# Optimization experiments

Measured on AMD Instinct MI355X. Metric: run time of the kernel, lower is better.

## Reference

```python
import jax, jax.numpy as jnp
import numpy as np

N_NODES = 100000
N_EDGES = 1600000
IN_F, HID_F, OUT_F = 64, 64, 16


def setup_inputs() -> dict:
    key = jax.random.key(0)
    k_x, k_e, k_w1, k_w2 = jax.random.split(key, 4)
    x = jax.random.normal(k_x, (N_NODES, IN_F), dtype=jnp.float32)
    edge_index = jax.random.randint(k_e, (2, N_EDGES), 0, N_NODES, dtype=jnp.int64)
    # Glorot-ish init for the GCNConv linear weights; bias zeros (PyG default)
    W1 = jax.random.normal(k_w1, (IN_F, HID_F), dtype=jnp.float32) / np.sqrt(IN_F)
    b1 = jnp.zeros((HID_F,), dtype=jnp.float32)
    W2 = jax.random.normal(k_w2, (HID_F, OUT_F), dtype=jnp.float32) / np.sqrt(HID_F)
    b2 = jnp.zeros((OUT_F,), dtype=jnp.float32)
    return {"x": x, "edge_index": edge_index, "W1": W1, "b1": b1, "W2": W2, "b2": b2}


def reference(x, edge_index, W1, b1, W2, b2):
    N = x.shape[0]
    # GCNConv: add self-loops, symmetric normalization D^-1/2 A D^-1/2
    loop = jnp.arange(N, dtype=edge_index.dtype)
    src = jnp.concatenate([edge_index[0], loop])  # [E+N]
    dst = jnp.concatenate([edge_index[1], loop])  # [E+N]
    deg = jax.ops.segment_sum(jnp.ones_like(dst, dtype=x.dtype), dst, num_segments=N)
    dis = jax.lax.rsqrt(deg)  # deg >= 1 due to self-loops
    norm = dis[src] * dis[dst]  # [E+N]

    def gcn_conv(h, W, b):
        h = h @ W                                   # [N, d_out]
        msg = h[src] * norm[:, None]                # gather + scale  [E+N, d_out]
        agg = jax.ops.segment_sum(msg, dst, num_segments=N)  # scatter-add
        return agg + b

    h = jax.nn.relu(gcn_conv(x, W1, b1))
    h = gcn_conv(h, W2, b2)
    return jax.nn.log_softmax(h, axis=1)
```

## Files before the change

kernel.cpp:

```cpp
#include <hip/hip_runtime.h>
#include <hip/hip_bf16.h>
#include <hip/hip_fp16.h>


#define F1 64
#define F2 16
#define NBKT 256
#define BSH 512
#define NSB 256
#define SBD 1024
#define STG 9216

typedef _Float16 f16x8 __attribute__((ext_vector_type(8)));
typedef _Float16 f16x4 __attribute__((ext_vector_type(4)));
typedef _Float16 f16x2 __attribute__((ext_vector_type(2)));
typedef float f32x4 __attribute__((ext_vector_type(4)));

__device__ inline f16x8 shfl_xor_f16x8(f16x8 v, int off) {
  union U { f16x8 h; int i[4]; } a, b;
  a.h = v;
#pragma unroll
  for (int k = 0; k < 4; ++k) b.i[k] = __shfl_xor(a.i[k], off);
  return b.h;
}
__device__ inline f16x4 shfl_xor_f16x4(f16x4 v, int off) {
  union U { f16x4 h; int i[2]; } a, b;
  a.h = v;
#pragma unroll
  for (int k = 0; k < 2; ++k) b.i[k] = __shfl_xor(a.i[k], off);
  return b.h;
}

__global__ void k_scatterL(const int* __restrict__ src, const int* __restrict__ dst,
                           int* __restrict__ tmp, int* __restrict__ segstart,
                           int* __restrict__ bcnt, int E, int nb, int chunk,
                           const float* __restrict__ W1, const float* __restrict__ W2,
                           __half* __restrict__ W1T, __half* __restrict__ W2T) {
  int t = threadIdx.x, sb = blockIdx.x;
  if (sb == NSB) {
    for (int i = t; i < 64 * 64; i += SBD) {
      int n = i >> 6, k = i & 63;
      W1T[i] = __float2half(W1[k * 64 + n]);
    }
    for (int i = t; i < 16 * 64; i += SBD) {
      int n = i >> 6, k = i & 63;
      W2T[i] = __float2half(W2[k * 16 + n]);
    }
    return;
  }
  __shared__ int h[NBKT];
  __shared__ int cur[NBKT];
  __shared__ int sc[NBKT];
  int beg = sb * chunk, end = min(beg + chunk, E);
  for (int i = t; i < NBKT; i += SBD) h[i] = 0;
  __syncthreads();
  int e;
  for (e = beg + t * 4; e + 4 <= end; e += 4 * SBD) {
    int4 d4 = *(const int4*)(dst + e);
    atomicAdd(&h[d4.x >> 9], 1);
    atomicAdd(&h[d4.y >> 9], 1);
    atomicAdd(&h[d4.z >> 9], 1);
    atomicAdd(&h[d4.w >> 9], 1);
  }
  for (; e < end; ++e) atomicAdd(&h[dst[e] >> 9], 1);
  __syncthreads();
  for (int i = t; i < nb; i += SBD)
    if (h[i]) atomicAdd(&bcnt[i], h[i]);
  if (t < NBKT) sc[t] = h[t];
  __syncthreads();
  for (int off = 1; off < NBKT; off <<= 1) {
    int a = (t < NBKT && t >= off) ? sc[t - off] : 0;
    __syncthreads();
    if (t < NBKT) sc[t] += a;
    __syncthreads();
  }
  if (t < NBKT) cur[t] = (t == 0) ? 0 : sc[t - 1];
  __syncthreads();
  for (int i = t; i < nb; i += SBD) segstart[sb * (nb + 1) + i] = beg + cur[i];
  if (t == 0) segstart[sb * (nb + 1) + nb] = end;
  __syncthreads();
  for (e = beg + t * 4; e + 4 <= end; e += 4 * SBD) {
    int4 d4 = *(const int4*)(dst + e);
    int4 s4 = *(const int4*)(src + e);
    int b, off;
    b = d4.x >> 9; off = atomicAdd(&cur[b], 1); tmp[beg + off] = (s4.x << 9) | (d4.x & 511);
    b = d4.y >> 9; off = atomicAdd(&cur[b], 1); tmp[beg + off] = (s4.y << 9) | (d4.y & 511);
    b = d4.z >> 9; off = atomicAdd(&cur[b], 1); tmp[beg + off] = (s4.z << 9) | (d4.z & 511);
    b = d4.w >> 9; off = atomicAdd(&cur[b], 1); tmp[beg + off] = (s4.w << 9) | (d4.w & 511);
  }
  for (; e < end; ++e) {
    int d = dst[e];
    int b = d >> 9;
    int off = atomicAdd(&cur[b], 1);
    tmp[beg + off] = (src[e] << 9) | (d & 511);
  }
}

__global__ void k_csr(const int* __restrict__ tmp, const int* __restrict__ segstart,
                      const int* __restrict__ bcnt, int* __restrict__ csr,
                      int* __restrict__ rowptr, float* __restrict__ dis,
                      int N, int nb) {
  __shared__ int stage[STG];
  __shared__ int sc[BSH];
  __shared__ int cnt[BSH];
  __shared__ int lofs[BSH];
  __shared__ int s_beg;
  int b = blockIdx.x, t = threadIdx.x;
  sc[t] = (t < b) ? bcnt[t] : 0;
  __syncthreads();
  for (int off = 1; off < BSH; off <<= 1) {
    int a = (t >= off) ? sc[t - off] : 0;
    __syncthreads();
    sc[t] += a;
    __syncthreads();
  }
  if (t == 0) s_beg = sc[BSH - 1];
  __syncthreads();
  int beg = s_beg;
  int s0 = 0, len = 0;
  if (t < NSB) {
    s0 = segstart[t * (nb + 1) + b];
    len = segstart[t * (nb + 1) + b + 1] - s0;
  }
  sc[t] = (t < NSB) ? len : 0;
  __syncthreads();
  for (int off = 1; off < NSB; off <<= 1) {
    int a = (t < NSB && t >= off) ? sc[t - off] : 0;
    __syncthreads();
    if (t < NSB) sc[t] += a;
    __syncthreads();
  }
  int total = sc[NSB - 1];
  int my0 = (t == 0) ? 0 : ((t < NSB) ? sc[t - 1] : 0);
  if (t < NSB) {
    int i = 0;
    for (; i + 4 <= len; i += 4) {
      int v0 = tmp[s0 + i], v1 = tmp[s0 + i + 1], v2 = tmp[s0 + i + 2], v3 = tmp[s0 + i + 3];
      stage[my0 + i] = v0; stage[my0 + i + 1] = v1;
      stage[my0 + i + 2] = v2; stage[my0 + i + 3] = v3;
    }
    for (; i < len; ++i) stage[my0 + i] = tmp[s0 + i];
  }
  cnt[t] = 0;
  __syncthreads();
  for (int i = t; i < total; i += BSH) atomicAdd(&cnt[stage[i] & (BSH - 1)], 1);
  __syncthreads();
  sc[t] = cnt[t];
  __syncthreads();
  for (int off = 1; off < BSH; off <<= 1) {
    int a = (t >= off) ? sc[t - off] : 0;
    __syncthreads();
    sc[t] += a;
    __syncthreads();
  }
  int excl = (t == 0) ? 0 : sc[t - 1];
  lofs[t] = excl;
  int n = b * BSH + t;
  if (n <= N) rowptr[n] = beg + excl;
  if (n < N) dis[n] = rsqrtf((float)(cnt[t] + 1));
  cnt[t] = 0;
  __syncthreads();
  for (int i = t; i < total; i += BSH) {
    int p = stage[i];
    int l = p & (BSH - 1);
    int off = atomicAdd(&cnt[l], 1);
    csr[beg + lofs[l] + off] = p >> 9;
  }
}

__global__ void k_gemm1(const float* __restrict__ x, const __half* __restrict__ W1T,
                        const float* __restrict__ dis, __half* __restrict__ out, int N) {
  int t = threadIdx.x;
  int wv = t >> 6, lane = t & 63;
  int m = lane & 15, q = lane >> 4;
  int row0 = blockIdx.x * 64 + wv * 16;
  int arow = min(row0 + m, N - 1);
  const _Float16* wt = (const _Float16*)W1T;
  f16x8 bf[4][2];
#pragma unroll
  for (int c = 0; c < 4; ++c)
#pragma unroll
    for (int kt = 0; kt < 2; ++kt)
      bf[c][kt] = *(const f16x8*)&wt[(c * 16 + m) * 64 + kt * 32 + q * 8];
  f16x8 a[2];
#pragma unroll
  for (int kt = 0; kt < 2; ++kt) {
    const float4* xp = (const float4*)(x + (size_t)arow * 64 + kt * 32 + q * 8);
    float4 u = xp[0], v = xp[1];
    a[kt][0] = (_Float16)u.x; a[kt][1] = (_Float16)u.y;
    a[kt][2] = (_Float16)u.z; a[kt][3] = (_Float16)u.w;
    a[kt][4] = (_Float16)v.x; a[kt][5] = (_Float16)v.y;
    a[kt][6] = (_Float16)v.z; a[kt][7] = (_Float16)v.w;
  }
  f32x4 acc[4] = {};
#pragma unroll
  for (int kt = 0; kt < 2; ++kt)
#pragma unroll
    for (int c = 0; c < 4; ++c)
      acc[c] = __builtin_amdgcn_mfma_f32_16x16x32_f16(a[kt], bf[c][kt], acc[c], 0, 0, 0);
#pragma unroll
  for (int r = 0; r < 4; ++r) {
    int n = row0 + q * 4 + r;
    if (n < N) {
      float dn = dis[n];
#pragma unroll
      for (int c = 0; c < 4; ++c)
        out[(size_t)n * 64 + c * 16 + m] = __float2half(acc[c][r] * dn);
    }
  }
}

__global__ void k_agg1f(const __half* __restrict__ h, const float* __restrict__ dis,
                        const int* __restrict__ rowptr, const int* __restrict__ csr,
                        const float* __restrict__ b1, const __half* __restrict__ W2T,
                        __half* __restrict__ h2, int N) {
  int gt = blockIdx.x * blockDim.x + threadIdx.x;
  int n = gt >> 6;
  if (n >= N) return;
  int lane = gt & 63;
  int fl = lane & 7;
  int sub = lane >> 3;
  const _Float16* hp = (const _Float16*)h;
  float dn = dis[n];
  float4 bu = *(const float4*)(b1 + fl * 8);
  float4 bv = *(const float4*)(b1 + fl * 8 + 4);
  const _Float16* wt = (const _Float16*)W2T;
  f16x8 w0 = *(const f16x8*)&wt[(sub * 2 + 0) * 64 + fl * 8];
  f16x8 w1 = *(const f16x8*)&wt[(sub * 2 + 1) * 64 + fl * 8];
  f16x8 acc0 = {}, acc1 = {};
  if (sub == 0)
    acc0 = *(const f16x8*)&hp[(size_t)n * 64 + fl * 8];
  int beg = rowptr[n], end = rowptr[n + 1];
  int e = beg + sub;
  int sA = (e < end) ? csr[e] : -1;
  int sB = (e + 8 < end) ? csr[e + 8] : -1;
  while (sB >= 0) {
    int e2 = e + 16;
    int sC = (e2 < end) ? csr[e2] : -1;
    int sD = (e2 + 8 < end) ? csr[e2 + 8] : -1;
    f16x8 v0 = *(const f16x8*)&hp[(size_t)sA * 64 + fl * 8];
    f16x8 v1 = *(const f16x8*)&hp[(size_t)sB * 64 + fl * 8];
    acc0 += v0;
    acc1 += v1;
    sA = sC; sB = sD; e = e2;
  }
  if (sA >= 0)
    acc0 += *(const f16x8*)&hp[(size_t)sA * 64 + fl * 8];
  f16x8 acc = acc0 + acc1;
  acc += shfl_xor_f16x8(acc, 8);
  acc += shfl_xor_f16x8(acc, 16);
  acc += shfl_xor_f16x8(acc, 32);
  float bb[8] = {bu.x, bu.y, bu.z, bu.w, bv.x, bv.y, bv.z, bv.w};
  f16x8 hr16;
#pragma unroll
  for (int k = 0; k < 8; ++k)
    hr16[k] = (_Float16)fmaxf(fmaf(dn, (float)acc[k], bb[k]), 0.f);
  const f16x2* h2v = (const f16x2*)&hr16;
  const f16x2* w0v = (const f16x2*)&w0;
  const f16x2* w1v = (const f16x2*)&w1;
  f16x2 q0 = {}, q1 = {};
#pragma unroll
  for (int k = 0; k < 4; ++k) {
    q0 += h2v[k] * w0v[k];
    q1 += h2v[k] * w1v[k];
  }
  float p0 = (float)q0[0] + (float)q0[1];
  float p1 = (float)q1[0] + (float)q1[1];
  p0 += __shfl_xor(p0, 1); p1 += __shfl_xor(p1, 1);
  p0 += __shfl_xor(p0, 2); p1 += __shfl_xor(p1, 2);
  p0 += __shfl_xor(p0, 4); p1 += __shfl_xor(p1, 4);
  if (fl == 0) {
    __half2 o;
    o.x = __float2half(p0 * dn);
    o.y = __float2half(p1 * dn);
    *(__half2*)((_Float16*)h2 + (size_t)n * 16 + sub * 2) = o;
  }
}

__global__ void k_agg2(const __half* __restrict__ h2, const float* __restrict__ dis,
                       const int* __restrict__ rowptr, const int* __restrict__ csr,
                       const float* __restrict__ b2, float* __restrict__ out, int N) {
  int gt = blockIdx.x * blockDim.x + threadIdx.x;
  int n = gt >> 6;
  if (n >= N) return;
  int lane = gt & 63;
  int fl = lane & 3;
  int sub = lane >> 2;
  const _Float16* hp = (const _Float16*)h2;
  f16x4 acc0 = {}, acc1 = {};
  if (sub == 0)
    acc0 = *(const f16x4*)&hp[(size_t)n * 16 + fl * 4];
  int beg = rowptr[n], end = rowptr[n + 1];
  int e = beg + sub;
  int sA = (e < end) ? csr[e] : -1;
  int sB = (e + 16 < end) ? csr[e + 16] : -1;
  while (sB >= 0) {
    int e2 = e + 32;
    int sC = (e2 < end) ? csr[e2] : -1;
    int sD = (e2 + 16 < end) ? csr[e2 + 16] : -1;
    f16x4 v0 = *(const f16x4*)&hp[(size_t)sA * 16 + fl * 4];
    f16x4 v1 = *(const f16x4*)&hp[(size_t)sB * 16 + fl * 4];
    acc0 += v0;
    acc1 += v1;
    sA = sC; sB = sD; e = e2;
  }
  if (sA >= 0)
    acc0 += *(const f16x4*)&hp[(size_t)sA * 16 + fl * 4];
  f16x4 acc = acc0 + acc1;
  acc += shfl_xor_f16x4(acc, 4);
  acc += shfl_xor_f16x4(acc, 8);
  acc += shfl_xor_f16x4(acc, 16);
  acc += shfl_xor_f16x4(acc, 32);
  if (sub == 0) {
    float dn = dis[n];
    float4 bb = *(const float4*)(b2 + fl * 4);
    float v0 = fmaf(dn, (float)acc[0], bb.x);
    float v1 = fmaf(dn, (float)acc[1], bb.y);
    float v2 = fmaf(dn, (float)acc[2], bb.z);
    float v3 = fmaf(dn, (float)acc[3], bb.w);
    float m = fmaxf(fmaxf(v0, v1), fmaxf(v2, v3));
    m = fmaxf(m, __shfl_xor(m, 1));
    m = fmaxf(m, __shfl_xor(m, 2));
    float s2 = __expf(v0 - m) + __expf(v1 - m) + __expf(v2 - m) + __expf(v3 - m);
    s2 += __shfl_xor(s2, 1);
    s2 += __shfl_xor(s2, 2);
    float ls = m + __logf(s2);
    float4 o = {v0 - ls, v1 - ls, v2 - ls, v3 - ls};
    *(float4*)(out + (size_t)n * 16 + fl * 4) = o;
  }
}

extern "C" void kernel_launch(void* const* d_in, const int* in_sizes, int n_in,
                              void* d_out, int out_size, void* d_ws, size_t ws_size,
                              hipStream_t stream) {
  const float* x = (const float*)d_in[0];
  const int* ei = (const int*)d_in[1];
  const float* W1 = (const float*)d_in[2];
  const float* b1 = (const float*)d_in[3];
  const float* W2 = (const float*)d_in[4];
  const float* b2 = (const float*)d_in[5];
  float* out = (float*)d_out;

  int N = in_sizes[0] / F1;
  int E = in_sizes[1] / 2;
  const int* src = ei;
  const int* dst = ei + E;
  int nb = (N + BSH - 1) >> 9;
  int chunk = ((E + NSB - 1) / NSB + 3) & ~3;

  char* ws = (char*)d_ws;
  size_t o_bcnt  = 0;
  size_t o_w1t   = o_bcnt + NBKT * 4;
  size_t o_w2t   = o_w1t + 64 * 64 * 2;
  size_t o_seg   = (o_w2t + 16 * 64 * 2 + 255) & ~(size_t)255;
  size_t o_dis   = (o_seg + (size_t)NSB * (nb + 1) * 4 + 255) & ~(size_t)255;
  size_t o_rowp  = (o_dis + (size_t)N * 4 + 255) & ~(size_t)255;
  size_t o_tmp   = (o_rowp + (size_t)(N + 1) * 4 + 255) & ~(size_t)255;
  size_t o_csr   = (o_tmp + (size_t)NSB * chunk * 4 + 255) & ~(size_t)255;
  size_t o_h1    = (o_csr + (size_t)E * 4 + 255) & ~(size_t)255;
  size_t o_h2    = (o_h1 + (size_t)N * 64 * 2 + 255) & ~(size_t)255;

  int* bcnt    = (int*)(ws + o_bcnt);
  __half* W1T  = (__half*)(ws + o_w1t);
  __half* W2T  = (__half*)(ws + o_w2t);
  int* segst   = (int*)(ws + o_seg);
  float* dis   = (float*)(ws + o_dis);
  int* rowptr  = (int*)(ws + o_rowp);
  int* tmp     = (int*)(ws + o_tmp);
  int* csr     = (int*)(ws + o_csr);
  __half* h1   = (__half*)(ws + o_h1);
  __half* h2   = (__half*)(ws + o_h2);

  hipMemsetAsync(bcnt, 0, NBKT * 4, stream);

  k_scatterL<<<NSB + 1, SBD, 0, stream>>>(src, dst, tmp, segst, bcnt, E, nb, chunk,
                                          W1, W2, W1T, W2T);
  k_csr<<<nb, BSH, 0, stream>>>(tmp, segst, bcnt, csr, rowptr, dis, N, nb);

  int gb = (N + 63) / 64;
  k_gemm1<<<gb, 256, 0, stream>>>(x, W1T, dis, h1, N);
  k_agg1f<<<((size_t)N * 64 + 255) / 256, 256, 0, stream>>>(h1, dis, rowptr, csr, b1, W2T, h2, N);
  k_agg2<<<((size_t)N * 64 + 255) / 256, 256, 0, stream>>>(h2, dis, rowptr, csr, b2, out, N);
}
```

Before: 200.7 us.

## Pack two nodes per wavefront in aggregation and derive bucket offsets from segstart

The two aggregation kernels now give each node half a wavefront (32 lanes) instead of a full one, so each wave handles two nodes. This halves the grid size and the shuffle-reduction depth, at the cost of fewer parallel edge lanes per node. Separately, the global per-bucket count array, its memset and its atomics are removed. k_csr instead recovers each bucket's global start by reducing segstart offsets minus each chunk base, which cuts one memset launch and the global atomic traffic.

```diff
diff --git a/kernel.cpp b/kernel.cpp
--- a/kernel.cpp
+++ b/kernel.cpp
@@ -33,7 +33,7 @@
 
 __global__ void k_scatterL(const int* __restrict__ src, const int* __restrict__ dst,
                            int* __restrict__ tmp, int* __restrict__ segstart,
-                           int* __restrict__ bcnt, int E, int nb, int chunk,
+                           int E, int nb, int chunk,
                            const float* __restrict__ W1, const float* __restrict__ W2,
                            __half* __restrict__ W1T, __half* __restrict__ W2T) {
   int t = threadIdx.x, sb = blockIdx.x;
@@ -64,8 +64,6 @@
   }
   for (; e < end; ++e) atomicAdd(&h[dst[e] >> 9], 1);
   __syncthreads();
-  for (int i = t; i < nb; i += SBD)
-    if (h[i]) atomicAdd(&bcnt[i], h[i]);
   if (t < NBKT) sc[t] = h[t];
   __syncthreads();
   for (int off = 1; off < NBKT; off <<= 1) {
@@ -97,31 +95,28 @@
 }
 
 __global__ void k_csr(const int* __restrict__ tmp, const int* __restrict__ segstart,
-                      const int* __restrict__ bcnt, int* __restrict__ csr,
-                      int* __restrict__ rowptr, float* __restrict__ dis,
-                      int N, int nb) {
+                      int* __restrict__ csr, int* __restrict__ rowptr,
+                      float* __restrict__ dis, int N, int nb, int chunk) {
   __shared__ int stage[STG];
   __shared__ int sc[BSH];
   __shared__ int cnt[BSH];
   __shared__ int lofs[BSH];
   __shared__ int s_beg;
   int b = blockIdx.x, t = threadIdx.x;
-  sc[t] = (t < b) ? bcnt[t] : 0;
-  __syncthreads();
-  for (int off = 1; off < BSH; off <<= 1) {
-    int a = (t >= off) ? sc[t - off] : 0;
-    __syncthreads();
-    sc[t] += a;
-    __syncthreads();
-  }
-  if (t == 0) s_beg = sc[BSH - 1];
-  __syncthreads();
-  int beg = s_beg;
   int s0 = 0, len = 0;
   if (t < NSB) {
     s0 = segstart[t * (nb + 1) + b];
     len = segstart[t * (nb + 1) + b + 1] - s0;
   }
+  sc[t] = (t < NSB) ? (s0 - t * chunk) : 0;
+  __syncthreads();
+  for (int off = BSH / 2; off > 0; off >>= 1) {
+    if (t < off) sc[t] += sc[t + off];
+    __syncthreads();
+  }
+  if (t == 0) s_beg = sc[0];
+  __syncthreads();
+  int beg = s_beg;
   sc[t] = (t < NSB) ? len : 0;
   __syncthreads();
   for (int off = 1; off < NSB; off <<= 1) {
@@ -215,21 +210,86 @@
                         const float* __restrict__ b1, const __half* __restrict__ W2T,
                         __half* __restrict__ h2, int N) {
   int gt = blockIdx.x * blockDim.x + threadIdx.x;
-  int n = gt >> 6;
+  int w = gt >> 6;
+  int lane = gt & 63;
+  int half = lane >> 5;
+  int sub = (lane >> 3) & 3;
+  int fl = lane & 7;
+  int n = w * 2 + half;
   if (n >= N) return;
-  int lane = gt & 63;
-  int fl = lane & 7;
-  int sub = lane >> 3;
   const _Float16* hp = (const _Float16*)h;
   float dn = dis[n];
   float4 bu = *(const float4*)(b1 + fl * 8);
   float4 bv = *(const float4*)(b1 + fl * 8 + 4);
   const _Float16* wt = (const _Float16*)W2T;
-  f16x8 w0 = *(const f16x8*)&wt[(sub * 2 + 0) * 64 + fl * 8];
-  f16x8 w1 = *(const f16x8*)&wt[(sub * 2 + 1) * 64 + fl * 8];
+  f16x8 wj[4];
+#pragma unroll
+  for (int i = 0; i < 4; ++i)
+    wj[i] = *(const f16x8*)&wt[(sub * 4 + i) * 64 + fl * 8];
   f16x8 acc0 = {}, acc1 = {};
   if (sub == 0)
     acc0 = *(const f16x8*)&hp[(size_t)n * 64 + fl * 8];
+  int beg = rowptr[n], end = rowptr[n + 1];
+  int e = beg + sub;
+  int sA = (e < end) ? csr[e] : -1;
+  int sB = (e + 4 < end) ? csr[e + 4] : -1;
+  while (sB >= 0) {
+    int e2 = e + 8;
+    int sC = (e2 < end) ? csr[e2] : -1;
+    int sD = (e2 + 4 < end) ? csr[e2 + 4] : -1;
+    f16x8 v0 = *(const f16x8*)&hp[(size_t)sA * 64 + fl * 8];
+    f16x8 v1 = *(const f16x8*)&hp[(size_t)sB * 64 + fl * 8];
+    acc0 += v0;
+    acc1 += v1;
+    sA = sC; sB = sD; e = e2;
+  }
+  if (sA >= 0)
+    acc0 += *(const f16x8*)&hp[(size_t)sA * 64 + fl * 8];
+  f16x8 acc = acc0 + acc1;
+  acc += shfl_xor_f16x8(acc, 8);
+  acc += shfl_xor_f16x8(acc, 16);
+  float bb[8] = {bu.x, bu.y, bu.z, bu.w, bv.x, bv.y, bv.z, bv.w};
+  f16x8 hr16;
+#pragma unroll
+  for (int k = 0; k < 8; ++k)
+    hr16[k] = (_Float16)fmaxf(fmaf(dn, (float)acc[k], bb[k]), 0.f);
+  const f16x2* h2v = (const f16x2*)&hr16;
+  float p[4];
+#pragma unroll
+  for (int i = 0; i < 4; ++i) {
+    const f16x2* wv = (const f16x2*)&wj[i];
+    f16x2 qq = {};
+#pragma unroll
+    for (int k = 0; k < 4; ++k) qq += h2v[k] * wv[k];
+    float pi = (float)qq[0] + (float)qq[1];
+    pi += __shfl_xor(pi, 1);
+    pi += __shfl_xor(pi, 2);
+    pi += __shfl_xor(pi, 4);
+    p[i] = pi;
+  }
+  if (fl == 0) {
+    f16x4 o;
+#pragma unroll
+    for (int i = 0; i < 4; ++i) o[i] = (_Float16)(p[i] * dn);
+    *(f16x4*)((_Float16*)h2 + (size_t)n * 16 + sub * 4) = o;
+  }
+}
+
+__global__ void k_agg2(const __half* __restrict__ h2, const float* __restrict__ dis,
+                       const int* __restrict__ rowptr, const int* __restrict__ csr,
+                       const float* __restrict__ b2, float* __restrict__ out, int N) {
+  int gt = blockIdx.x * blockDim.x + threadIdx.x;
+  int w = gt >> 6;
+  int lane = gt & 63;
+  int half = lane >> 5;
+  int sub = (lane >> 2) & 7;
+  int fl = lane & 3;
+  int n = w * 2 + half;
+  if (n >= N) return;
+  const _Float16* hp = (const _Float16*)h2;
+  f16x4 acc0 = {}, acc1 = {};
+  if (sub == 0)
+    acc0 = *(const f16x4*)&hp[(size_t)n * 16 + fl * 4];
   int beg = rowptr[n], end = rowptr[n + 1];
   int e = beg + sub;
   int sA = (e < end) ? csr[e] : -1;
@@ -238,66 +298,6 @@
     int e2 = e + 16;
     int sC = (e2 < end) ? csr[e2] : -1;
     int sD = (e2 + 8 < end) ? csr[e2 + 8] : -1;
-    f16x8 v0 = *(const f16x8*)&hp[(size_t)sA * 64 + fl * 8];
-    f16x8 v1 = *(const f16x8*)&hp[(size_t)sB * 64 + fl * 8];
-    acc0 += v0;
-    acc1 += v1;
-    sA = sC; sB = sD; e = e2;
-  }
-  if (sA >= 0)
-    acc0 += *(const f16x8*)&hp[(size_t)sA * 64 + fl * 8];
-  f16x8 acc = acc0 + acc1;
-  acc += shfl_xor_f16x8(acc, 8);
-  acc += shfl_xor_f16x8(acc, 16);
-  acc += shfl_xor_f16x8(acc, 32);
-  float bb[8] = {bu.x, bu.y, bu.z, bu.w, bv.x, bv.y, bv.z, bv.w};
-  f16x8 hr16;
-#pragma unroll
-  for (int k = 0; k < 8; ++k)
-    hr16[k] = (_Float16)fmaxf(fmaf(dn, (float)acc[k], bb[k]), 0.f);
-  const f16x2* h2v = (const f16x2*)&hr16;
-  const f16x2* w0v = (const f16x2*)&w0;
-  const f16x2* w1v = (const f16x2*)&w1;
-  f16x2 q0 = {}, q1 = {};
-#pragma unroll
-  for (int k = 0; k < 4; ++k) {
-    q0 += h2v[k] * w0v[k];
-    q1 += h2v[k] * w1v[k];
-  }
-  float p0 = (float)q0[0] + (float)q0[1];
-  float p1 = (float)q1[0] + (float)q1[1];
-  p0 += __shfl_xor(p0, 1); p1 += __shfl_xor(p1, 1);
-  p0 += __shfl_xor(p0, 2); p1 += __shfl_xor(p1, 2);
-  p0 += __shfl_xor(p0, 4); p1 += __shfl_xor(p1, 4);
-  if (fl == 0) {
-    __half2 o;
-    o.x = __float2half(p0 * dn);
-    o.y = __float2half(p1 * dn);
-    *(__half2*)((_Float16*)h2 + (size_t)n * 16 + sub * 2) = o;
-  }
-}
-
-__global__ void k_agg2(const __half* __restrict__ h2, const float* __restrict__ dis,
-                       const int* __restrict__ rowptr, const int* __restrict__ csr,
-                       const float* __restrict__ b2, float* __restrict__ out, int N) {
-  int gt = blockIdx.x * blockDim.x + threadIdx.x;
-  int n = gt >> 6;
-  if (n >= N) return;
-  int lane = gt & 63;
-  int fl = lane & 3;
-  int sub = lane >> 2;
-  const _Float16* hp = (const _Float16*)h2;
-  f16x4 acc0 = {}, acc1 = {};
-  if (sub == 0)
-    acc0 = *(const f16x4*)&hp[(size_t)n * 16 + fl * 4];
-  int beg = rowptr[n], end = rowptr[n + 1];
-  int e = beg + sub;
-  int sA = (e < end) ? csr[e] : -1;
-  int sB = (e + 16 < end) ? csr[e + 16] : -1;
-  while (sB >= 0) {
-    int e2 = e + 32;
-    int sC = (e2 < end) ? csr[e2] : -1;
-    int sD = (e2 + 16 < end) ? csr[e2 + 16] : -1;
     f16x4 v0 = *(const f16x4*)&hp[(size_t)sA * 16 + fl * 4];
     f16x4 v1 = *(const f16x4*)&hp[(size_t)sB * 16 + fl * 4];
     acc0 += v0;
@@ -310,7 +310,6 @@
   acc += shfl_xor_f16x4(acc, 4);
   acc += shfl_xor_f16x4(acc, 8);
   acc += shfl_xor_f16x4(acc, 16);
-  acc += shfl_xor_f16x4(acc, 32);
   if (sub == 0) {
     float dn = dis[n];
     float4 bb = *(const float4*)(b2 + fl * 4);
@@ -349,8 +348,7 @@
   int chunk = ((E + NSB - 1) / NSB + 3) & ~3;
 
   char* ws = (char*)d_ws;
-  size_t o_bcnt  = 0;
-  size_t o_w1t   = o_bcnt + NBKT * 4;
+  size_t o_w1t   = 0;
   size_t o_w2t   = o_w1t + 64 * 64 * 2;
   size_t o_seg   = (o_w2t + 16 * 64 * 2 + 255) & ~(size_t)255;
   size_t o_dis   = (o_seg + (size_t)NSB * (nb + 1) * 4 + 255) & ~(size_t)255;
@@ -360,7 +358,6 @@
   size_t o_h1    = (o_csr + (size_t)E * 4 + 255) & ~(size_t)255;
   size_t o_h2    = (o_h1 + (size_t)N * 64 * 2 + 255) & ~(size_t)255;
 
-  int* bcnt    = (int*)(ws + o_bcnt);
   __half* W1T  = (__half*)(ws + o_w1t);
   __half* W2T  = (__half*)(ws + o_w2t);
   int* segst   = (int*)(ws + o_seg);
@@ -371,14 +368,13 @@
   __half* h1   = (__half*)(ws + o_h1);
   __half* h2   = (__half*)(ws + o_h2);
 
-  hipMemsetAsync(bcnt, 0, NBKT * 4, stream);
-
-  k_scatterL<<<NSB + 1, SBD, 0, stream>>>(src, dst, tmp, segst, bcnt, E, nb, chunk,
+  k_scatterL<<<NSB + 1, SBD, 0, stream>>>(src, dst, tmp, segst, E, nb, chunk,
                                           W1, W2, W1T, W2T);
-  k_csr<<<nb, BSH, 0, stream>>>(tmp, segst, bcnt, csr, rowptr, dis, N, nb);
+  k_csr<<<nb, BSH, 0, stream>>>(tmp, segst, csr, rowptr, dis, N, nb, chunk);
 
   int gb = (N + 63) / 64;
   k_gemm1<<<gb, 256, 0, stream>>>(x, W1T, dis, h1, N);
-  k_agg1f<<<((size_t)N * 64 + 255) / 256, 256, 0, stream>>>(h1, dis, rowptr, csr, b1, W2T, h2, N);
-  k_agg2<<<((size_t)N * 64 + 255) / 256, 256, 0, stream>>>(h2, dis, rowptr, csr, b2, out, N);
-}
+  int aw = (N + 1) / 2;
+  k_agg1f<<<((size_t)aw * 64 + 255) / 256, 256, 0, stream>>>(h1, dis, rowptr, csr, b1, W2T, h2, N);
+  k_agg2<<<((size_t)aw * 64 + 255) / 256, 256, 0, stream>>>(h2, dis, rowptr, csr, b2, out, N);
+}
```

Result: faster. 174.0 us (median of 2 runs) (-13.3%).
